# Kernel tuning notes

Hardware: AMD Instinct MI355X
Metric: run time of the kernel (lower is better)

## Reference

```python
import jax, jax.numpy as jnp
import numpy as np
from jax import lax

GN_EPS = 1e-5
LRELU_SLOPE = 0.2
TOP_K = 3
COMMITMENT = 0.25
NUM_CODES = 1024

def conv(x, w, b, stride=1, pad=1):
    y = lax.conv_general_dilated(x, w, (stride, stride), ((pad, pad), (pad, pad)),
                                 dimension_numbers=('NCHW', 'OIHW', 'NCHW'))
    return y + b[None, :, None, None]

def conv_transpose(x, w, b, stride=2, pad=1, out_pad=1):
    # torch ConvTranspose2d: w is (Cin, Cout, kH, kW); equivalent to lhs-dilated conv
    # with flipped, io-swapped kernel and padding k-1-p (plus out_pad on high side).
    k = w.shape[2]
    p = k - 1 - pad
    w_f = jnp.transpose(jnp.flip(w, (2, 3)), (1, 0, 2, 3))  # -> OIHW
    y = lax.conv_general_dilated(x, w_f, (1, 1), ((p, p + out_pad), (p, p + out_pad)),
                                 lhs_dilation=(stride, stride),
                                 dimension_numbers=('NCHW', 'OIHW', 'NCHW'))
    return y + b[None, :, None, None]

def group_norm(x, g, beta, groups=2):
    N, C, H, W = x.shape
    xg = x.reshape(N, groups, C // groups, H, W)
    mu = xg.mean((2, 3, 4), keepdims=True)
    var = xg.var((2, 3, 4), keepdims=True)
    xn = ((xg - mu) * lax.rsqrt(var + GN_EPS)).reshape(N, C, H, W)
    return xn * g[None, :, None, None] + beta[None, :, None, None]

def lrelu(x):
    return jnp.where(x >= 0, x, LRELU_SLOPE * x)

def vq_ema_eval(z, emb):
    # z: [B, D, H, W] -> tokens [N, D]; eval path (no EMA buffer updates)
    inputs = jnp.transpose(z, (0, 2, 3, 1))  # [B,H,W,D]
    flat = inputs.reshape(-1, emb.shape[1])
    d = (jnp.sum(flat ** 2, 1, keepdims=True) + jnp.sum(emb ** 2, 1)
         - 2.0 * flat @ emb.T)  # [N, K]
    _, idx = lax.top_k(-d, TOP_K)  # top_k smallest distances
    q0 = emb[idx[:, 0]].reshape(inputs.shape)
    e_latent_loss = jnp.mean((lax.stop_gradient(q0) - inputs) ** 2)
    loss = COMMITMENT * e_latent_loss
    quantized = inputs + lax.stop_gradient(q0 - inputs)  # straight-through
    # perplexity uses the LAST (k-th nearest) encodings, matching the torch loop
    last = idx[:, TOP_K - 1]
    counts = jnp.zeros((emb.shape[0],), flat.dtype).at[last].add(1.0)
    avg_probs = counts / flat.shape[0]
    perplexity = jnp.exp(-jnp.sum(avg_probs * jnp.log(avg_probs + 1e-10)))
    return loss, jnp.transpose(quantized, (0, 3, 1, 2)), perplexity

def setup_inputs() -> dict:
    key = jax.random.key(0)
    ks = jax.random.split(key, 16)
    s = 0.05
    d = {
        'x': jax.random.normal(ks[0], (4, 4, 96, 96), jnp.float32),
        'e0_w': jax.random.normal(ks[1], (128, 4, 3, 3), jnp.float32) * s,
        'e0_b': jnp.zeros((128,), jnp.float32),
        'e0_g': jnp.ones((128,), jnp.float32),
        'e0_beta': jnp.zeros((128,), jnp.float32),
        'e1_w': jax.random.normal(ks[2], (128, 128, 3, 3), jnp.float32) * s,
        'e1_b': jnp.zeros((128,), jnp.float32),
        'e1_g': jnp.ones((128,), jnp.float32),
        'e1_beta': jnp.zeros((128,), jnp.float32),
        'pv_w': jax.random.normal(ks[3], (128, 128, 1, 1), jnp.float32) * s,
        'pv_b': jnp.zeros((128,), jnp.float32),
        'emb': jax.random.normal(ks[4], (NUM_CODES, 128), jnp.float32),
        'd0_w': jax.random.normal(ks[5], (128, 128, 3, 3), jnp.float32) * s,  # ConvT: (Cin,Cout,k,k)
        'd0_b': jnp.zeros((128,), jnp.float32),
        'd0_g': jnp.ones((128,), jnp.float32),
        'd0_beta': jnp.zeros((128,), jnp.float32),
        'd1_w': jax.random.normal(ks[6], (128, 256, 3, 3), jnp.float32) * s,
        'd1_b': jnp.zeros((128,), jnp.float32),
        'd1_g': jnp.ones((128,), jnp.float32),
        'd1_beta': jnp.zeros((128,), jnp.float32),
        'proj_w': jax.random.normal(ks[7], (128, 128, 1, 1), jnp.float32) * s,
        'proj_b': jnp.zeros((128,), jnp.float32),
        'ro_w': jax.random.normal(ks[8], (4, 128, 1, 1), jnp.float32) * s,
        'ro_b': jnp.zeros((4,), jnp.float32),
    }
    return d

def reference(x, e0_w, e0_b, e0_g, e0_beta, e1_w, e1_b, e1_g, e1_beta,
              pv_w, pv_b, emb,
              d0_w, d0_b, d0_g, d0_beta, d1_w, d1_b, d1_g, d1_beta,
              proj_w, proj_b, ro_w, ro_b):
    # Encoder: strides [1, 2]
    enc1 = lrelu(group_norm(conv(x, e0_w, e0_b, stride=1, pad=1), e0_g, e0_beta))
    latent = lrelu(group_norm(conv(enc1, e1_w, e1_b, stride=2, pad=1), e1_g, e1_beta))
    z = conv(latent, pv_w, pv_b, stride=1, pad=0)
    loss, quantized, perplexity = vq_ema_eval(z, emb)
    # Decoder: strides [2, 1]; skip projected (embedding_dim != C_out)
    skip = conv(enc1, proj_w, proj_b, stride=1, pad=0)
    h = lrelu(group_norm(conv_transpose(quantized, d0_w, d0_b, stride=2, pad=1, out_pad=1), d0_g, d0_beta))
    y = lrelu(group_norm(conv(jnp.concatenate([h, skip], axis=1), d1_w, d1_b, stride=1, pad=1), d1_g, d1_beta))
    x_recon = conv(y, ro_w, ro_b, stride=1, pad=0)
    return (loss, x_recon, perplexity)
```

## Files before the change

kernel.cpp:

```cpp
#include <hip/hip_runtime.h>

#define DEVI __device__ __forceinline__

typedef unsigned short u16;
typedef __attribute__((ext_vector_type(8))) short bf8v;
typedef __attribute__((ext_vector_type(4))) short s4v;
typedef __attribute__((ext_vector_type(4))) float f4v;

constexpr int NB = 4, C = 128, H = 96, W = 96, HW = H * W;
constexpr int HL = 48, WL = 48, HWL = HL * WL;
constexpr int CODES = 1024, DIM = 128;
constexpr int ROWS = NB * HWL;

DEVI float lrelu_f(float v) { return v >= 0.f ? v : 0.2f * v; }

DEVI u16 f2bf(float f) {
  union { float f; unsigned u; } v; v.f = f;
  unsigned r = (v.u + 0x7FFFu + ((v.u >> 16) & 1u)) >> 16;
  return (u16)r;
}

DEVI float bf2f(u16 h) {
  union { unsigned u; float f; } v; v.u = (unsigned)h << 16;
  return v.f;
}

DEVI void wave_red2(float& s, float& s2) {
#pragma unroll
  for (int o = 32; o > 0; o >>= 1) { s += __shfl_down(s, o); s2 += __shfl_down(s2, o); }
}

DEVI bool block_red2(float& s, float& s2) {
  wave_red2(s, s2);
  __shared__ float ls[8], ls2[8];
  int wv = threadIdx.x >> 6, ln = threadIdx.x & 63;
  if (ln == 0) { ls[wv] = s; ls2[wv] = s2; }
  __syncthreads();
  if (threadIdx.x == 0) {
    s = ls[0] + ls[1] + ls[2] + ls[3];
    s2 = ls2[0] + ls2[1] + ls2[2] + ls2[3];
    return true;
  }
  return false;
}

DEVI void ins3(float e, int j, float& d0, int& i0, float& d1, int& i1, float& d2, int& i2) {
  bool b0 = (e < d0) || (e == d0 && j < i0);
  bool b1 = (e < d1) || (e == d1 && j < i1);
  bool b2 = (e < d2) || (e == d2 && j < i2);
  float nd0 = b0 ? e : d0;             int ni0 = b0 ? j : i0;
  float nd1 = b0 ? d0 : (b1 ? e : d1); int ni1 = b0 ? i0 : (b1 ? j : i1);
  float nd2 = b1 ? d1 : (b2 ? e : d2); int ni2 = b1 ? i1 : (b2 ? j : i2);
  d0 = nd0; i0 = ni0; d1 = nd1; i1 = ni1; d2 = nd2; i2 = ni2;
}

__global__ __launch_bounds__(256) void k_red16(const float2* __restrict__ src,
                                               float* __restrict__ dst, int per) {
  int slot = blockIdx.x;
  float s = 0.f, s2 = 0.f;
  for (int i = threadIdx.x; i < per; i += 256) {
    float2 v = src[(size_t)slot * per + i];
    s += v.x; s2 += v.y;
  }
  if (block_red2(s, s2)) { dst[slot * 2] = s; dst[slot * 2 + 1] = s2; }
}

__global__ __launch_bounds__(256) void k_pack_all(
    const float* __restrict__ d1_w, const float* __restrict__ d0_w,
    const float* __restrict__ pj_w, const float* __restrict__ emb,
    u16* __restrict__ A1, u16* __restrict__ A0, u16* __restrict__ Apj,
    u16* __restrict__ ehtil, float* __restrict__ enorm, float* __restrict__ counts) {
  int b = blockIdx.x, t = threadIdx.x;
  if (b < 1152) {
    int i = b * 256 + t;
    int ci = i & 31, co = (i >> 5) & 127, r = i >> 12;
    int kx = r % 3; int r2 = r / 3; int ch = r2 & 7, ky = r2 >> 3;
    A1[i] = f2bf(d1_w[((size_t)(co * 256 + ch * 32 + ci) * 3 + ky) * 3 + kx]);
  } else if (b < 1728) {
    int i = (b - 1152) * 256 + t;
    int ci = i & 31, co = (i >> 5) & 127, r = i >> 12;
    int wx = r % 3; int r2 = r / 3; int ch = r2 & 3, wy = r2 >> 2;
    A0[i] = f2bf(d0_w[((size_t)((ch * 32 + ci) * 128 + co) * 3 + wy) * 3 + wx]);
  } else if (b < 1792) {
    int i = (b - 1728) * 256 + t;
    int ci = i & 31, co = (i >> 5) & 127, ch = i >> 12;
    Apj[i] = f2bf(pj_w[co * 128 + ch * 32 + ci]);
  } else if (b < 1920) {
    int g = (b - 1792) * 256 + t;
    int ct = g >> 9; int rem = g & 511;
    int j = rem >> 6; int l = rem & 63;
    int code = ct * 16 + (l & 15);
    int kb = j * 32 + (l >> 4) * 8;
    bool lo = kb >= 128; int k0 = lo ? kb - 128 : kb;
    const float* ep = emb + (size_t)code * DIM + k0;
    u16 o[8];
#pragma unroll
    for (int e = 0; e < 8; ++e) {
      float v = ep[e];
      u16 h = f2bf(v);
      o[e] = lo ? f2bf(v - bf2f(h)) : h;
    }
    bf8v ov = {(short)o[0], (short)o[1], (short)o[2], (short)o[3],
               (short)o[4], (short)o[5], (short)o[6], (short)o[7]};
    *(bf8v*)&ehtil[(size_t)g * 8] = ov;
  } else if (b < 1924) {
    int e = (b - 1920) * 256 + t;
    const float4* p = (const float4*)(emb + (size_t)e * DIM);
    float s = 0.f;
#pragma unroll 8
    for (int i = 0; i < 32; ++i) {
      float4 v = p[i];
      s = fmaf(v.x, v.x, s); s = fmaf(v.y, v.y, s); s = fmaf(v.z, v.z, s); s = fmaf(v.w, v.w, s);
    }
    enorm[e] = s;
  } else {
#pragma unroll
    for (int k = 0; k < 4; ++k) counts[t + k * 256] = 0.f;
  }
}

__global__ __launch_bounds__(256) void k_conv_e0t(
    const float* __restrict__ x, const float* __restrict__ wg,
    const float* __restrict__ bias, float* __restrict__ out, float2* __restrict__ ps) {
  __shared__ float xs[4][18][104];
  int b = blockIdx.x;
  int rq = b % 6; int co = (b / 6) & 127; int n = b / 768;
  int t = threadIdx.x;
  int tx = t & 15, r = t >> 4;
  int y0 = rq * 16;
  for (int e = t; e < 4 * 18 * 104; e += 256) {
    int ci = e / 1872; int rem = e - ci * 1872;
    int row = rem / 104; int off = rem - row * 104;
    int iy = y0 - 1 + row; int ix = off - 1;
    float v = 0.f;
    if ((unsigned)iy < 96u && (unsigned)ix < 96u)
      v = x[((size_t)(n * 4 + ci)) * HW + iy * 96 + ix];
    xs[ci][row][off] = v;
  }
  float wr[4][9];
  const float* wp = wg + co * 36;
#pragma unroll
  for (int ci = 0; ci < 4; ++ci)
#pragma unroll
    for (int k = 0; k < 9; ++k) wr[ci][k] = wp[ci * 9 + k];
  float bv = bias[co];
  __syncthreads();
  float acc[6];
#pragma unroll
  for (int p = 0; p < 6; ++p) acc[p] = bv;
#pragma unroll
  for (int ci = 0; ci < 4; ++ci) {
#pragma unroll
    for (int ky = 0; ky < 3; ++ky) {
      const float* rp = &xs[ci][r + ky][6 * tx];
      float f[8];
#pragma unroll
      for (int j = 0; j < 4; ++j) {
        float2 v2 = *(const float2*)(rp + 2 * j);
        f[2 * j] = v2.x; f[2 * j + 1] = v2.y;
      }
      float w0 = wr[ci][ky * 3 + 0], w1 = wr[ci][ky * 3 + 1], w2 = wr[ci][ky * 3 + 2];
#pragma unroll
      for (int p = 0; p < 6; ++p)
        acc[p] = fmaf(w0, f[p], fmaf(w1, f[p + 1], fmaf(w2, f[p + 2], acc[p])));
    }
  }
  float* op = out + ((size_t)(n * 128 + co) * 96 + (y0 + r)) * 96 + 6 * tx;
#pragma unroll
  for (int j = 0; j < 3; ++j) {
    float2 v2 = { acc[2 * j], acc[2 * j + 1] };
    *(float2*)(op + 2 * j) = v2;
  }
  float s = 0.f, s2 = 0.f;
#pragma unroll
  for (int p = 0; p < 6; ++p) { s += acc[p]; s2 += acc[p] * acc[p]; }
  if (block_red2(s, s2)) {
    int slot = n * 2 + (co >> 6);
    ps[(size_t)slot * 384 + (co & 63) * 6 + rq] = make_float2(s, s2);
  }
}

__global__ __launch_bounds__(256) void k_gn_pad(
    const float* __restrict__ in, const float* __restrict__ stats,
    const float* __restrict__ gam, const float* __restrict__ bet, float* __restrict__ outp) {
  int idx = blockIdx.x * 256 + threadIdx.x;
  int col = idx % 100; int r2 = idx / 100; int row = r2 % 98; int c2 = r2 / 98;
  int c = c2 & 127; int n = c2 >> 7;
  float v = 0.f;
  if (row >= 1 && row <= 96 && col >= 1 && col <= 96) {
    const float* st = stats + (n * 2 + (c >> 6)) * 2;
    const float invc = 1.f / (64.f * 9216.f);
    float mu = st[0] * invc;
    float var = fmaf(-mu, mu, st[1] * invc);
    float rs = rsqrtf(var + 1e-5f);
    float raw = in[(size_t)c2 * 9216 + (row - 1) * 96 + (col - 1)];
    v = lrelu_f(fmaf((raw - mu) * rs, gam[c], bet[c]));
  }
  outp[idx] = v;
}

__global__ __launch_bounds__(256) void k_gn_nhwc_bf(
    const float* __restrict__ in, u16* __restrict__ outb, const float* __restrict__ stats,
    const float* __restrict__ gam, const float* __restrict__ bet) {
  int idx = blockIdx.x * 256 + threadIdx.x;
  int c = idx & 127;
  int n = idx / (9216 * 128);
  const float* st = stats + (n * 2 + (c >> 6)) * 2;
  const float invcnt = 1.f / (64.f * 9216.f);
  float mu = st[0] * invcnt;
  float var = fmaf(-mu, mu, st[1] * invcnt);
  float rs = rsqrtf(var + 1e-5f);
  float v = in[idx];
  outb[idx] = f2bf(lrelu_f(fmaf((v - mu) * rs, gam[c], bet[c])));
}

__global__ __launch_bounds__(256, 4) void k_conv_e1s(
    const float* __restrict__ gnpad, const float* __restrict__ wg, float* __restrict__ part) {
  __shared__ float insh[8 * 500];
  __shared__ float wsh[8 * 576];
  int b = blockIdx.x;
  int cb = b & 1; int kb = (b >> 1) & 3; int rq = (b >> 3) % 24; int n = b / 192;
  int co0 = cb * 64;
  int t = threadIdx.x;
  int tx = t & 15, r = (t >> 4) & 1, cg = t >> 5;
  float acc[8][3];
#pragma unroll
  for (int c = 0; c < 8; ++c)
#pragma unroll
    for (int p = 0; p < 3; ++p) acc[c][p] = 0.f;
  for (int cc = 0; cc < 4; ++cc) {
    __syncthreads();
    const float4* src = (const float4*)(gnpad + ((size_t)(n * 128 + kb * 32 + cc * 8)) * 9800 + 4 * rq * 100);
#pragma unroll
    for (int j = 0; j < 4; ++j) {
      int e = t + j * 256;
      if (e < 1000) {
        int ci = e / 125; int q = e - ci * 125;
        *(float4*)&insh[ci * 500 + q * 4] = src[(size_t)ci * 2450 + q];
      }
    }
#pragma unroll
    for (int j = 0; j < 18; ++j) {
      int e = t + j * 256;
      int ci = e / 576; int rem = e - ci * 576; int k = rem >> 6; int co = rem & 63;
      wsh[e] = wg[(size_t)(co0 + co) * 1152 + (kb * 32 + cc * 8 + ci) * 9 + k];
    }
    __syncthreads();
#pragma unroll
    for (int ci = 0; ci < 8; ++ci) {
      float iv[3][3][3];
      int ib = ci * 500 + (2 * r) * 100 + 2 * tx;
#pragma unroll
      for (int ky = 0; ky < 3; ++ky) {
#pragma unroll
        for (int p = 0; p < 3; ++p) {
          int a = ib + ky * 100 + 32 * p;
          float2 v2 = *(const float2*)&insh[a];
          iv[ky][p][0] = v2.x; iv[ky][p][1] = v2.y; iv[ky][p][2] = insh[a + 2];
        }
      }
#pragma unroll
      for (int k = 0; k < 9; ++k) {
        float4 wa = *(const float4*)&wsh[ci * 576 + k * 64 + cg * 8];
        float4 wb = *(const float4*)&wsh[ci * 576 + k * 64 + cg * 8 + 4];
        int ky = k / 3, kx = k - ky * 3;
#pragma unroll
        for (int p = 0; p < 3; ++p) {
          float ivv = iv[ky][p][kx];
          acc[0][p] = fmaf(wa.x, ivv, acc[0][p]);
          acc[1][p] = fmaf(wa.y, ivv, acc[1][p]);
          acc[2][p] = fmaf(wa.z, ivv, acc[2][p]);
          acc[3][p] = fmaf(wa.w, ivv, acc[3][p]);
          acc[4][p] = fmaf(wb.x, ivv, acc[4][p]);
          acc[5][p] = fmaf(wb.y, ivv, acc[5][p]);
          acc[6][p] = fmaf(wb.z, ivv, acc[6][p]);
          acc[7][p] = fmaf(wb.w, ivv, acc[7][p]);
        }
      }
    }
  }
  int oy = 2 * rq + r;
#pragma unroll
  for (int c = 0; c < 8; ++c) {
    size_t ob = (size_t)kb * 1179648 + ((size_t)(n * 128 + co0 + cg * 8 + c)) * HWL + oy * 48 + tx;
#pragma unroll
    for (int p = 0; p < 3; ++p) part[ob + 16 * p] = acc[c][p];
  }
}

__global__ __launch_bounds__(256) void k_e1comb(
    const float* __restrict__ part, const float* __restrict__ bias,
    float* __restrict__ latent, float2* __restrict__ ps) {
  int idx = blockIdx.x * 256 + threadIdx.x;
  int c = (idx / HWL) & 127;
  int n = idx / (HWL * 128);
  float v = part[idx] + part[idx + 1179648] + part[idx + 2 * 1179648] + part[idx + 3 * 1179648] + bias[c];
  latent[idx] = v;
  float s = v, s2 = v * v;
  if (block_red2(s, s2)) {
    int slot = n * 2 + (c >> 6);
    int j = blockIdx.x % 9;
    ps[(size_t)slot * 576 + (c & 63) * 9 + j] = make_float2(s, s2);
  }
}

__global__ __launch_bounds__(256, 2) void k_pv(
    const float* __restrict__ in, const float* __restrict__ w,
    const float* __restrict__ bias, const float* __restrict__ stats1,
    const float* __restrict__ gam, const float* __restrict__ bet,
    u16* __restrict__ zp) {
  int b = blockIdx.x;
  int pxb = b % 36; int cb = (b / 36) & 1; int n = b / 72;
  int t = threadIdx.x;
  int pxg = t & 7, cg = t >> 3;
  int px0 = pxb * 64 + pxg * 8;
  int cobase = cb * 64 + cg * 2;
  const float invc = 1.f / (64.f * 2304.f);
  float acc[2][8];
#pragma unroll
  for (int c = 0; c < 2; ++c) {
    float bv = bias[cobase + c];
#pragma unroll
    for (int p = 0; p < 8; ++p) acc[c][p] = bv;
  }
  const float* ipb = in + (size_t)n * 128 * HWL + px0;
  for (int ci0 = 0; ci0 < 128; ci0 += 4) {
    float inr[4][8];
#pragma unroll
    for (int i = 0; i < 4; ++i) {
      int c = ci0 + i;
      const float* st = stats1 + (n * 2 + (c >> 6)) * 2;
      float mu = st[0] * invc;
      float var = fmaf(-mu, mu, st[1] * invc);
      float rsv = rsqrtf(var + 1e-5f);
      float ga = gam[c], be = bet[c];
      const float* ip = ipb + (size_t)c * HWL;
      float4 a = *(const float4*)ip; float4 bq = *(const float4*)(ip + 4);
      inr[i][0] = lrelu_f(fmaf((a.x - mu) * rsv, ga, be));
      inr[i][1] = lrelu_f(fmaf((a.y - mu) * rsv, ga, be));
      inr[i][2] = lrelu_f(fmaf((a.z - mu) * rsv, ga, be));
      inr[i][3] = lrelu_f(fmaf((a.w - mu) * rsv, ga, be));
      inr[i][4] = lrelu_f(fmaf((bq.x - mu) * rsv, ga, be));
      inr[i][5] = lrelu_f(fmaf((bq.y - mu) * rsv, ga, be));
      inr[i][6] = lrelu_f(fmaf((bq.z - mu) * rsv, ga, be));
      inr[i][7] = lrelu_f(fmaf((bq.w - mu) * rsv, ga, be));
    }
    float wr[2][4];
#pragma unroll
    for (int c = 0; c < 2; ++c) {
      float4 wv = *(const float4*)&w[(size_t)(cobase + c) * 128 + ci0];
      wr[c][0] = wv.x; wr[c][1] = wv.y; wr[c][2] = wv.z; wr[c][3] = wv.w;
    }
#pragma unroll
    for (int i = 0; i < 4; ++i)
#pragma unroll
      for (int c = 0; c < 2; ++c)
#pragma unroll
        for (int p = 0; p < 8; ++p) acc[c][p] = fmaf(wr[c][i], inr[i][p], acc[c][p]);
  }
#pragma unroll
  for (int p = 0; p < 8; ++p) {
    size_t r = (size_t)n * HWL + px0 + p;
    u16 h0 = f2bf(acc[0][p]); u16 l0 = f2bf(acc[0][p] - bf2f(h0));
    u16 h1 = f2bf(acc[1][p]); u16 l1 = f2bf(acc[1][p] - bf2f(h1));
    unsigned hp = (unsigned)h0 | ((unsigned)h1 << 16);
    unsigned lp = (unsigned)l0 | ((unsigned)l1 << 16);
    *(unsigned*)&zp[r * 256 + cobase] = hp;
    *(unsigned*)&zp[r * 256 + 128 + cobase] = lp;
  }
}

__global__ __launch_bounds__(1024, 1) void k_vq(
    const u16* __restrict__ zp, const u16* __restrict__ ehtil,
    const float* __restrict__ emb, const float* __restrict__ enorm,
    u16* __restrict__ qb, float* __restrict__ counts, float* __restrict__ pvq) {
  __shared__ float wd[16][16][3];
  __shared__ int   wi[16][16][3];
  __shared__ float lred[16];
  __shared__ int hist[CODES];
  int r0 = blockIdx.x * 16;
  int t = threadIdx.x, w = t >> 6, lane = t & 63;
  int ln16 = lane & 15, quad = lane >> 4;
  hist[t] = 0;
  const u16* zrow = zp + (size_t)(r0 + ln16) * 256 + quad * 8;
  bf8v bh[4], bl[4];
#pragma unroll
  for (int kk = 0; kk < 4; ++kk) {
    bh[kk] = *(const bf8v*)(zrow + kk * 32);
    bl[kk] = *(const bf8v*)(zrow + 128 + kk * 32);
  }
  float d0 = 3.4e38f, d1 = 3.4e38f, d2 = 3.4e38f;
  int i0 = -1, i1 = -1, i2 = -1;
  const u16* abase = ehtil + (size_t)(w * 4) * 4096 + lane * 8;
#pragma unroll
  for (int tt = 0; tt < 4; ++tt) {
    const u16* ap = abase + tt * 4096;
    bf8v af[8];
#pragma unroll
    for (int j = 0; j < 8; ++j) af[j] = *(const bf8v*)(ap + j * 512);
    f4v accA = (f4v){0.f, 0.f, 0.f, 0.f};
    f4v accB = (f4v){0.f, 0.f, 0.f, 0.f};
    f4v accC = (f4v){0.f, 0.f, 0.f, 0.f};
#pragma unroll
    for (int kk = 0; kk < 4; ++kk) {
      accA = __builtin_amdgcn_mfma_f32_16x16x32_bf16(af[kk], bh[kk], accA, 0, 0, 0);
      accB = __builtin_amdgcn_mfma_f32_16x16x32_bf16(af[4 + kk], bh[kk], accB, 0, 0, 0);
      accC = __builtin_amdgcn_mfma_f32_16x16x32_bf16(af[kk], bl[kk], accC, 0, 0, 0);
    }
    int cbase = (w * 4 + tt) * 16 + quad * 4;
#pragma unroll
    for (int g = 0; g < 4; ++g) {
      int code = cbase + g;
      float dot = accA[g] + accB[g] + accC[g];
      float d = fmaf(-2.f, dot, enorm[code]);
      bool b0 = d < d0, b1 = d < d1, b2 = d < d2;
      float nd0 = b0 ? d : d0;             int ni0 = b0 ? code : i0;
      float nd1 = b0 ? d0 : (b1 ? d : d1); int ni1 = b0 ? i0 : (b1 ? code : i1);
      float nd2 = b1 ? d1 : (b2 ? d : d2); int ni2 = b1 ? i1 : (b2 ? code : i2);
      d0 = nd0; i0 = ni0; d1 = nd1; i1 = ni1; d2 = nd2; i2 = ni2;
    }
  }
#pragma unroll
  for (int off = 16; off <= 32; off <<= 1) {
    float e0 = __shfl_xor(d0, off), e1 = __shfl_xor(d1, off), e2 = __shfl_xor(d2, off);
    int j0 = __shfl_xor(i0, off), j1 = __shfl_xor(i1, off), j2 = __shfl_xor(i2, off);
    ins3(e0, j0, d0, i0, d1, i1, d2, i2);
    ins3(e1, j1, d0, i0, d1, i1, d2, i2);
    ins3(e2, j2, d0, i0, d1, i1, d2, i2);
  }
  if (quad == 0) {
    wd[w][ln16][0] = d0; wd[w][ln16][1] = d1; wd[w][ln16][2] = d2;
    wi[w][ln16][0] = i0; wi[w][ln16][1] = i1; wi[w][ln16][2] = i2;
  }
  __syncthreads();
  float bd; int bi;
  if (lane < 48) { bd = wd[lane / 3][w][lane % 3]; bi = wi[lane / 3][w][lane % 3]; }
  else { bd = 3.4e38f; bi = 0x7fffffff; }
  int a[3];
#pragma unroll
  for (int p = 0; p < 3; ++p) {
    float d = bd; int i = bi;
#pragma unroll
    for (int o = 1; o <= 32; o <<= 1) {
      float od = __shfl_xor(d, o); int oi = __shfl_xor(i, o);
      if (od < d || (od == d && oi < i)) { d = od; i = oi; }
    }
    a[p] = i;
    if (bi == i) { bd = 3.4e38f; bi = 0x7fffffff; }
  }
  int r = r0 + w;
  const float* q0p = emb + (size_t)a[0] * DIM;
  const u16* zr = zp + (size_t)r * 256;
  float lp = 0.f;
#pragma unroll
  for (int cc = 0; cc < 2; ++cc) {
    int c = lane + cc * 64;
    float qv = q0p[c];
    qb[(size_t)r * 128 + c] = f2bf(qv);
    float zv = bf2f(zr[c]) + bf2f(zr[128 + c]);
    float dd = zv - qv;
    lp = fmaf(dd, dd, lp);
  }
#pragma unroll
  for (int o = 32; o > 0; o >>= 1) lp += __shfl_down(lp, o);
  if (lane == 0) { lred[w] = lp; atomicAdd(&hist[a[2]], 1); }
  __syncthreads();
  if (t == 0) {
    float s = 0.f;
#pragma unroll
    for (int q = 0; q < 16; ++q) s += lred[q];
    pvq[blockIdx.x] = s;
  }
  int cnt = hist[t];
  if (cnt) atomicAdd(&counts[t], (float)cnt);
}

__global__ __launch_bounds__(256) void k_finalize(
    const float* __restrict__ counts, const float* __restrict__ pvq, float* __restrict__ out) {
  float local = 0.f;
#pragma unroll
  for (int k = 0; k < 4; ++k) {
    float cnt = counts[threadIdx.x + k * 256];
    float pr = cnt * (1.f / (float)ROWS);
    local = fmaf(pr, logf(pr + 1e-10f), local);
  }
  float lsum = 0.f;
  for (int i = threadIdx.x; i < ROWS / 16; i += 256) lsum += pvq[i];
  if (block_red2(local, lsum)) {
    out[1 + NB * 4 * HW] = expf(-local);
    out[0] = 0.25f * lsum * (1.f / (9216.f * 128.f));
  }
}

__global__ __launch_bounds__(256) void k_proj_m(
    const float* __restrict__ enc1, const u16* __restrict__ Apj,
    const float* __restrict__ bias, const float* __restrict__ stats0,
    const float* __restrict__ gam, const float* __restrict__ bet,
    u16* __restrict__ skipb) {
  __shared__ u16 Ash[128 * 32];
  __shared__ u16 Bsh[96 * 32];
  int b = blockIdx.x; int rowi = b % 96; int n = b / 96; int px0 = rowi * 96;
  int t = threadIdx.x; int w = t >> 6; int lane = t & 63;
  int ln16 = lane & 15, quad = lane >> 4;
  int co0w = (w & 1) * 64; int pxh = (w >> 1) * 48;
  int c_l = t & 31, xg = t >> 5;
  const float invc = 1.f / (64.f * 9216.f);
  f4v acc[4][3];
#pragma unroll
  for (int mt = 0; mt < 4; ++mt)
#pragma unroll
    for (int nt = 0; nt < 3; ++nt) acc[mt][nt] = (f4v){0.f, 0.f, 0.f, 0.f};
  for (int ch = 0; ch < 4; ++ch) {
    __syncthreads();
#pragma unroll
    for (int e = 0; e < 2; ++e) {
      int i = t + e * 256;
      *(bf8v*)&Ash[i * 8] = *(const bf8v*)&Apj[ch * 4096 + i * 8];
    }
    int c = ch * 32 + c_l;
    const float* st = stats0 + (n * 2 + (ch >> 1)) * 2;
    float mu = st[0] * invc;
    float var = fmaf(-mu, mu, st[1] * invc);
    float rsv = rsqrtf(var + 1e-5f);
    float ga = gam[c], be = bet[c];
    const float* ip = enc1 + (size_t)(n * 128 + c) * 9216 + px0 + xg * 12;
#pragma unroll
    for (int j4 = 0; j4 < 3; ++j4) {
      float4 v = *(const float4*)(ip + j4 * 4);
      int pxb = xg * 12 + j4 * 4;
      Bsh[(pxb + 0) * 32 + c_l] = f2bf(lrelu_f(fmaf((v.x - mu) * rsv, ga, be)));
      Bsh[(pxb + 1) * 32 + c_l] = f2bf(lrelu_f(fmaf((v.y - mu) * rsv, ga, be)));
      Bsh[(pxb + 2) * 32 + c_l] = f2bf(lrelu_f(fmaf((v.z - mu) * rsv, ga, be)));
      Bsh[(pxb + 3) * 32 + c_l] = f2bf(lrelu_f(fmaf((v.w - mu) * rsv, ga, be)));
    }
    __syncthreads();
    bf8v af[4];
#pragma unroll
    for (int mt = 0; mt < 4; ++mt)
      af[mt] = *(const bf8v*)&Ash[(co0w + mt * 16 + ln16) * 32 + quad * 8];
#pragma unroll
    for (int nt = 0; nt < 3; ++nt) {
      bf8v bfv = *(const bf8v*)&Bsh[(pxh + nt * 16 + ln16) * 32 + quad * 8];
#pragma unroll
      for (int mt = 0; mt < 4; ++mt)
        acc[mt][nt] = __builtin_amdgcn_mfma_f32_16x16x32_bf16(af[mt], bfv, acc[mt][nt], 0, 0, 0);
    }
  }
#pragma unroll
  for (int mt = 0; mt < 4; ++mt) {
    int co = co0w + mt * 16 + quad * 4;
    float4 bv = *(const float4*)&bias[co];
#pragma unroll
    for (int nt = 0; nt < 3; ++nt) {
      int px = px0 + pxh + nt * 16 + ln16;
      u16* dp = skipb + (size_t)(n * 9216 + px) * 128 + co;
      s4v sv;
      sv.x = (short)f2bf(acc[mt][nt].x + bv.x);
      sv.y = (short)f2bf(acc[mt][nt].y + bv.y);
      sv.z = (short)f2bf(acc[mt][nt].z + bv.z);
      sv.w = (short)f2bf(acc[mt][nt].w + bv.w);
      *(s4v*)dp = sv;
    }
  }
}

__global__ __launch_bounds__(256) void k_convt_d0m(
    const u16* __restrict__ qb, const u16* __restrict__ A0,
    const float* __restrict__ bias, float* __restrict__ h, float2* __restrict__ ps) {
  __shared__ u16 Ash[2 * 128 * 32];
  __shared__ u16 Bsh[49 * 32];
  int b = blockIdx.x; int rx = b & 1; int oy = (b >> 1) % 96; int n = b / 192;
  int t = threadIdx.x; int w = t >> 6; int lane = t & 63;
  int ln16 = lane & 15, quad = lane >> 4;
  int co0w = w * 32;
  f4v acc[2][3];
#pragma unroll
  for (int mt = 0; mt < 2; ++mt)
#pragma unroll
    for (int nt = 0; nt < 3; ++nt) acc[mt][nt] = (f4v){0.f, 0.f, 0.f, 0.f};
  int nyt, wys[2], iys[2];
  if (oy & 1) {
    wys[0] = 2; iys[0] = (oy - 1) >> 1;
    wys[1] = 0; iys[1] = (oy + 1) >> 1;
    nyt = (iys[1] < 48) ? 2 : 1;
  } else { wys[0] = 1; iys[0] = oy >> 1; wys[1] = 0; iys[1] = 0; nyt = 1; }
  int nxt = rx ? 2 : 1;
  int wxs[2], xof[2];
  if (rx) { wxs[0] = 2; xof[0] = 0; wxs[1] = 0; xof[1] = 1; }
  else { wxs[0] = 1; xof[0] = 0; wxs[1] = 0; xof[1] = 0; }
  for (int yt = 0; yt < nyt; ++yt) {
    for (int ch = 0; ch < 4; ++ch) {
      __syncthreads();
      for (int e = t; e < nxt * 512; e += 256) {
        int xt = e >> 9, e2 = e & 511;
        const u16* Asrc = A0 + (size_t)(((wys[yt] * 4 + ch) * 3 + wxs[xt]) * 4096);
        *(bf8v*)&Ash[xt * 4096 + e2 * 8] = *(const bf8v*)&Asrc[e2 * 8];
      }
      const u16* bbase = qb + (size_t)(n * 2304 + iys[yt] * 48) * 128 + ch * 32;
      for (int e = t; e < 196; e += 256) {
        int row = e >> 2, seg = e & 3;
        bf8v v = {0, 0, 0, 0, 0, 0, 0, 0};
        if (row < 48) v = *(const bf8v*)&bbase[row * 128 + seg * 8];
        *(bf8v*)&Bsh[row * 32 + seg * 8] = v;
      }
      __syncthreads();
      for (int xt = 0; xt < nxt; ++xt) {
        bf8v af[2];
#pragma unroll
        for (int mt = 0; mt < 2; ++mt)
          af[mt] = *(const bf8v*)&Ash[xt * 4096 + (co0w + mt * 16 + ln16) * 32 + quad * 8];
#pragma unroll
        for (int nt = 0; nt < 3; ++nt) {
          bf8v bfv = *(const bf8v*)&Bsh[(nt * 16 + ln16 + xof[xt]) * 32 + quad * 8];
#pragma unroll
          for (int mt = 0; mt < 2; ++mt)
            acc[mt][nt] = __builtin_amdgcn_mfma_f32_16x16x32_bf16(af[mt], bfv, acc[mt][nt], 0, 0, 0);
        }
      }
    }
  }
  float s = 0.f, s2 = 0.f;
#pragma unroll
  for (int mt = 0; mt < 2; ++mt) {
    int co = co0w + mt * 16 + quad * 4;
    float4 bv = *(const float4*)&bias[co];
#pragma unroll
    for (int nt = 0; nt < 3; ++nt) {
      int px = nt * 16 + ln16;
      int ox = 2 * px + rx;
      float4 v;
      v.x = acc[mt][nt].x + bv.x; v.y = acc[mt][nt].y + bv.y;
      v.z = acc[mt][nt].z + bv.z; v.w = acc[mt][nt].w + bv.w;
      *(float4*)(h + (size_t)(n * 9216 + oy * 96 + ox) * 128 + co) = v;
      s += v.x + v.y + v.z + v.w;
      s2 += v.x * v.x + v.y * v.y + v.z * v.z + v.w * v.w;
    }
  }
  wave_red2(s, s2);
  if (lane == 0) {
    int slot = n * 2 + (w >> 1);
    ps[(size_t)slot * 384 + (oy * 2 + rx) * 2 + (w & 1)] = make_float2(s, s2);
  }
}

__global__ __launch_bounds__(256) void k_conv_d1m(
    const u16* __restrict__ hb, const u16* __restrict__ sb,
    const u16* __restrict__ A1, const float* __restrict__ bias,
    float* __restrict__ y, float2* __restrict__ ps) {
  __shared__ u16 Ash[3 * 64 * 32];
  __shared__ u16 Bsh[98 * 32];
  int b = blockIdx.x; int cb = b & 1; int oy = (b >> 1) % 96; int n = b / 192;
  int t = threadIdx.x; int w = t >> 6; int lane = t & 63;
  int ln16 = lane & 15, quad = lane >> 4;
  int co0w = (w & 1) * 32; int pxh = (w >> 1) * 48;
  f4v acc[2][3];
#pragma unroll
  for (int mt = 0; mt < 2; ++mt)
#pragma unroll
    for (int nt = 0; nt < 3; ++nt) acc[mt][nt] = (f4v){0.f, 0.f, 0.f, 0.f};
  int ky0 = (oy == 0) ? 1 : 0, ky1 = (oy == 95) ? 1 : 2;
  for (int ky = ky0; ky <= ky1; ++ky) {
    int iy = oy + ky - 1;
    for (int ch = 0; ch < 8; ++ch) {
      const u16* src = (ch < 4) ? hb : sb;
      int c0 = (ch & 3) * 32;
      const u16* Asrc = A1 + (size_t)(ky * 8 + ch) * 12288;
      const u16* bbase = src + (size_t)(n * 9216 + iy * 96) * 128 + c0;
      __syncthreads();
#pragma unroll
      for (int j = 0; j < 3; ++j) {
        int e = t + j * 256;
        int kx = e >> 8; int e2 = e & 255; int co_l = e2 >> 2; int seg = e2 & 3;
        *(bf8v*)&Ash[(kx * 64 + co_l) * 32 + seg * 8] =
            *(const bf8v*)&Asrc[(size_t)kx * 4096 + (cb * 64 + co_l) * 32 + seg * 8];
      }
      for (int e = t; e < 392; e += 256) {
        int row = e >> 2, seg = e & 3;
        int ix = row - 1;
        bf8v v = {0, 0, 0, 0, 0, 0, 0, 0};
        if ((unsigned)ix < 96u) v = *(const bf8v*)&bbase[ix * 128 + seg * 8];
        *(bf8v*)&Bsh[row * 32 + seg * 8] = v;
      }
      __syncthreads();
#pragma unroll
      for (int kx = 0; kx < 3; ++kx) {
        bf8v af[2];
#pragma unroll
        for (int mt = 0; mt < 2; ++mt)
          af[mt] = *(const bf8v*)&Ash[(kx * 64 + co0w + mt * 16 + ln16) * 32 + quad * 8];
#pragma unroll
        for (int nt = 0; nt < 3; ++nt) {
          bf8v bfv = *(const bf8v*)&Bsh[(pxh + nt * 16 + ln16 + kx) * 32 + quad * 8];
#pragma unroll
          for (int mt = 0; mt < 2; ++mt)
            acc[mt][nt] = __builtin_amdgcn_mfma_f32_16x16x32_bf16(af[mt], bfv, acc[mt][nt], 0, 0, 0);
        }
      }
    }
  }
  float s = 0.f, s2 = 0.f;
#pragma unroll
  for (int mt = 0; mt < 2; ++mt) {
    int co = cb * 64 + co0w + mt * 16 + quad * 4;
    float4 bv = *(const float4*)&bias[co];
#pragma unroll
    for (int nt = 0; nt < 3; ++nt) {
      int px = pxh + nt * 16 + ln16;
      float4 v;
      v.x = acc[mt][nt].x + bv.x; v.y = acc[mt][nt].y + bv.y;
      v.z = acc[mt][nt].z + bv.z; v.w = acc[mt][nt].w + bv.w;
      *(float4*)(y + (size_t)(n * 9216 + oy * 96 + px) * 128 + co) = v;
      s += v.x + v.y + v.z + v.w;
      s2 += v.x * v.x + v.y * v.y + v.z * v.z + v.w * v.w;
    }
  }
  wave_red2(s, s2);
  if (lane == 0) {
    int slot = n * 2 + cb;
    ps[(size_t)slot * 384 + oy * 4 + w] = make_float2(s, s2);
  }
}

__global__ __launch_bounds__(256) void k_ro(
    const float* __restrict__ y, const float* __restrict__ w,
    const float* __restrict__ bias, const float* __restrict__ stats3,
    const float* __restrict__ gam, const float* __restrict__ bet,
    float* __restrict__ out) {
  __shared__ float wsh[512];
  __shared__ float gsh[128], bsh[128];
  __shared__ float red[64][16];
  int b = blockIdx.x; int n = b / 144; int px0 = (b % 144) * 64;
  int t = threadIdx.x; int q = t & 3, pxl = t >> 2;
  for (int e = t; e < 512; e += 256) wsh[e] = w[e];
  if (t < 128) { gsh[t] = gam[t]; bsh[t] = bet[t]; }
  __syncthreads();
  const float invc = 1.f / (64.f * 9216.f);
  int g = q >> 1;
  const float* st = stats3 + (n * 2 + g) * 2;
  float mu = st[0] * invc;
  float var = fmaf(-mu, mu, st[1] * invc);
  float rsv = rsqrtf(var + 1e-5f);
  const float* yb = y + (size_t)(n * 9216 + px0 + pxl) * 128 + q * 32;
  float s0 = 0.f, s1 = 0.f, s2 = 0.f, s3 = 0.f;
#pragma unroll
  for (int j = 0; j < 8; ++j) {
    float4 v = *(const float4*)(yb + j * 4);
    int c0 = q * 32 + j * 4;
    float vx = lrelu_f(fmaf((v.x - mu) * rsv, gsh[c0 + 0], bsh[c0 + 0]));
    float vy = lrelu_f(fmaf((v.y - mu) * rsv, gsh[c0 + 1], bsh[c0 + 1]));
    float vz = lrelu_f(fmaf((v.z - mu) * rsv, gsh[c0 + 2], bsh[c0 + 2]));
    float vw = lrelu_f(fmaf((v.w - mu) * rsv, gsh[c0 + 3], bsh[c0 + 3]));
    const float* w0 = &wsh[0 * 128 + c0];
    const float* w1 = &wsh[1 * 128 + c0];
    const float* w2 = &wsh[2 * 128 + c0];
    const float* w3 = &wsh[3 * 128 + c0];
    s0 += vx * w0[0] + vy * w0[1] + vz * w0[2] + vw * w0[3];
    s1 += vx * w1[0] + vy * w1[1] + vz * w1[2] + vw * w1[3];
    s2 += vx * w2[0] + vy * w2[1] + vz * w2[2] + vw * w2[3];
    s3 += vx * w3[0] + vy * w3[1] + vz * w3[2] + vw * w3[3];
  }
  red[pxl][q * 4 + 0] = s0; red[pxl][q * 4 + 1] = s1;
  red[pxl][q * 4 + 2] = s2; red[pxl][q * 4 + 3] = s3;
  __syncthreads();
  float val = red[pxl][0 * 4 + q] + red[pxl][1 * 4 + q] + red[pxl][2 * 4 + q] + red[pxl][3 * 4 + q] + bias[q];
  out[1 + (size_t)(n * 4 + q) * 9216 + px0 + pxl] = val;
}

extern "C" void kernel_launch(void* const* d_in, const int* in_sizes, int n_in,
                              void* d_out, int out_size, void* d_ws, size_t ws_size,
                              hipStream_t stream) {
  (void)in_sizes; (void)n_in; (void)out_size; (void)ws_size;
  const float* x     = (const float*)d_in[0];
  const float* e0_w  = (const float*)d_in[1];
  const float* e0_b  = (const float*)d_in[2];
  const float* e0_g  = (const float*)d_in[3];
  const float* e0_bt = (const float*)d_in[4];
  const float* e1_w  = (const float*)d_in[5];
  const float* e1_b  = (const float*)d_in[6];
  const float* e1_g  = (const float*)d_in[7];
  const float* e1_bt = (const float*)d_in[8];
  const float* pv_w  = (const float*)d_in[9];
  const float* pv_b  = (const float*)d_in[10];
  const float* emb   = (const float*)d_in[11];
  const float* d0_w  = (const float*)d_in[12];
  const float* d0_b  = (const float*)d_in[13];
  const float* d0_g  = (const float*)d_in[14];
  const float* d0_bt = (const float*)d_in[15];
  const float* d1_w  = (const float*)d_in[16];
  const float* d1_b  = (const float*)d_in[17];
  const float* d1_g  = (const float*)d_in[18];
  const float* d1_bt = (const float*)d_in[19];
  const float* pj_w  = (const float*)d_in[20];
  const float* pj_b  = (const float*)d_in[21];
  const float* ro_w  = (const float*)d_in[22];
  const float* ro_b  = (const float*)d_in[23];
  float* out = (float*)d_out;
  float* ws = (float*)d_ws;

  float* stats  = ws;
  float* counts = ws + 64;
  float* enorm  = ws + 1088;
  float* pvq    = ws + 2112;
  float2* ps_e0 = (float2*)(ws + 3264);
  float2* ps_e1 = (float2*)(ws + 76992);
  float2* ps_d0 = (float2*)(ws + 95424);
  float2* ps_d1 = (float2*)(ws + 107712);
  float* enc1   = ws + 114688;
  float* latent = enc1 + (size_t)NB * C * HW;
  float* zbuf   = latent + (size_t)NB * C * HWL;
  float* hy     = zbuf + (size_t)NB * C * HWL;
  u16* qb    = (u16*)(hy + (size_t)NB * C * HW);
  u16* hb    = qb + (size_t)NB * C * HWL;
  u16* skipb = hb + (size_t)NB * C * HW;
  u16* A1    = skipb + (size_t)NB * C * HW;
  u16* A0    = A1 + 294912;
  u16* Apj   = A0 + 147456;
  u16* ehtil = Apj + 16384 + 64;
  u16* zp    = (u16*)zbuf;
  float* gnpad = (float*)qb;

  k_pack_all<<<1925, 256, 0, stream>>>(d1_w, d0_w, pj_w, emb, A1, A0, Apj, ehtil, enorm, counts);

  k_conv_e0t<<<3072, 256, 0, stream>>>(x, e0_w, e0_b, enc1, ps_e0);
  k_red16<<<8, 256, 0, stream>>>(ps_e0, stats + 0, 384);
  k_gn_pad<<<512 * 9800 / 256, 256, 0, stream>>>(enc1, stats + 0, e0_g, e0_bt, gnpad);
  k_conv_e1s<<<768, 256, 0, stream>>>(gnpad, e1_w, hy);
  k_e1comb<<<NB * C * HWL / 256, 256, 0, stream>>>(hy, e1_b, latent, ps_e1);
  k_red16<<<8, 256, 0, stream>>>(ps_e1, stats + 16, 576);
  k_pv<<<288, 256, 0, stream>>>(latent, pv_w, pv_b, stats + 16, e1_g, e1_bt, zp);
  k_vq<<<ROWS / 16, 1024, 0, stream>>>(zp, ehtil, emb, enorm, qb, counts, pvq);
  k_finalize<<<1, 256, 0, stream>>>(counts, pvq, out);

  k_proj_m<<<NB * 96, 256, 0, stream>>>(enc1, Apj, pj_b, stats + 0, e0_g, e0_bt, skipb);
  k_convt_d0m<<<NB * 96 * 2, 256, 0, stream>>>(qb, A0, d0_b, hy, ps_d0);
  k_red16<<<8, 256, 0, stream>>>(ps_d0, stats + 32, 384);
  k_gn_nhwc_bf<<<NB * C * HW / 256, 256, 0, stream>>>(hy, hb, stats + 32, d0_g, d0_bt);
  k_conv_d1m<<<NB * 96 * 2, 256, 0, stream>>>(hb, skipb, A1, d1_b, hy, ps_d1);
  k_red16<<<8, 256, 0, stream>>>(ps_d1, stats + 48, 384);
  k_ro<<<NB * 144, 256, 0, stream>>>(hy, ro_w, ro_b, stats + 48, d1_g, d1_bt, out);
}
```

Baseline: 384.0 us.

## Move encoder stride-2 conv to split-bf16 MFMA with packed NHWC input

Replaces the FP32 split-K direct conv for the second encoder layer, and its separate combine kernel, with an MFMA kernel. Precision is kept by splitting values into hi/lo bf16 parts and issuing three MFMAs per product. The group-norm pass now writes channel-blocked, even/odd-column-deinterleaved bf16 hi/lo rows, and weights are pre-packed in the pack kernel. Bias, the latent store and the partial statistics are fused into the conv epilogue, which removes the partial-sum buffer traffic and one launch. The cost is three times the MFMA work plus rounding error from the split-bf16 approximation.

```diff
diff --git a/kernel.cpp b/kernel.cpp
--- a/kernel.cpp
+++ b/kernel.cpp
@@ -68,8 +68,10 @@
 __global__ __launch_bounds__(256) void k_pack_all(
     const float* __restrict__ d1_w, const float* __restrict__ d0_w,
     const float* __restrict__ pj_w, const float* __restrict__ emb,
+    const float* __restrict__ e1_w,
     u16* __restrict__ A1, u16* __restrict__ A0, u16* __restrict__ Apj,
-    u16* __restrict__ ehtil, float* __restrict__ enorm, float* __restrict__ counts) {
+    u16* __restrict__ ehtil, u16* __restrict__ We1,
+    float* __restrict__ enorm, float* __restrict__ counts) {
   int b = blockIdx.x, t = threadIdx.x;
   if (b < 1152) {
     int i = b * 256 + t;
@@ -113,9 +115,27 @@
       s = fmaf(v.x, v.x, s); s = fmaf(v.y, v.y, s); s = fmaf(v.z, v.z, s); s = fmaf(v.w, v.w, s);
     }
     enorm[e] = s;
+  } else if (b == 1924) {
+#pragma unroll
+    for (int k = 0; k < 4; ++k) counts[t + k * 256] = 0.f;
   } else {
-#pragma unroll
-    for (int k = 0; k < 4; ++k) counts[t + k * 256] = 0.f;
+    int p = (b - 1925) * 256 + t;
+    int s = p >> 6, l = p & 63;
+    int ct = s & 7; int r = s >> 3;
+    int kx = r % 3; int r2 = r / 3; int ch = r2 & 3, ky = r2 >> 2;
+    int co = ct * 16 + (l & 15), ci0 = ch * 32 + (l >> 4) * 8;
+    u16 hh[8], ll[8];
+#pragma unroll
+    for (int e = 0; e < 8; ++e) {
+      float v = e1_w[((size_t)(co * 128 + ci0 + e) * 3 + ky) * 3 + kx];
+      u16 h = f2bf(v); hh[e] = h; ll[e] = f2bf(v - bf2f(h));
+    }
+    bf8v hv = {(short)hh[0], (short)hh[1], (short)hh[2], (short)hh[3],
+               (short)hh[4], (short)hh[5], (short)hh[6], (short)hh[7]};
+    bf8v lv = {(short)ll[0], (short)ll[1], (short)ll[2], (short)ll[3],
+               (short)ll[4], (short)ll[5], (short)ll[6], (short)ll[7]};
+    *(bf8v*)&We1[(size_t)s * 1024 + l * 8] = hv;
+    *(bf8v*)&We1[(size_t)s * 1024 + 512 + l * 8] = lv;
   }
 }
 
@@ -180,23 +200,116 @@
   }
 }
 
-__global__ __launch_bounds__(256) void k_gn_pad(
-    const float* __restrict__ in, const float* __restrict__ stats,
-    const float* __restrict__ gam, const float* __restrict__ bet, float* __restrict__ outp) {
-  int idx = blockIdx.x * 256 + threadIdx.x;
-  int col = idx % 100; int r2 = idx / 100; int row = r2 % 98; int c2 = r2 / 98;
-  int c = c2 & 127; int n = c2 >> 7;
-  float v = 0.f;
-  if (row >= 1 && row <= 96 && col >= 1 && col <= 96) {
-    const float* st = stats + (n * 2 + (c >> 6)) * 2;
-    const float invc = 1.f / (64.f * 9216.f);
-    float mu = st[0] * invc;
-    float var = fmaf(-mu, mu, st[1] * invc);
-    float rs = rsqrtf(var + 1e-5f);
-    float raw = in[(size_t)c2 * 9216 + (row - 1) * 96 + (col - 1)];
-    v = lrelu_f(fmaf((raw - mu) * rs, gam[c], bet[c]));
-  }
-  outp[idx] = v;
+__global__ __launch_bounds__(256) void k_gn_px(
+    const float* __restrict__ enc1, const float* __restrict__ stats,
+    const float* __restrict__ gam, const float* __restrict__ bet, u16* __restrict__ xp) {
+  int b = blockIdx.x;
+  int ch = b & 3; int iy = (b >> 2) % 96; int n = b / 384;
+  int t = threadIdx.x;
+  const float invc = 1.f / (64.f * 9216.f);
+  size_t chunk = ((size_t)((n * 96 + iy) * 4 + ch)) * 6208;
+  for (int e = t; e < 388; e += 256) {
+    int oct = e / 97, u = e - oct * 97;
+    int ix = (u < 48) ? 2 * u : 2 * (u - 48) - 1;
+    u16* dh = xp + chunk + u * 32 + oct * 8;
+    u16* dl = dh + 3104;
+    if (ix < 0) {
+      bf8v z = {0, 0, 0, 0, 0, 0, 0, 0};
+      *(bf8v*)dh = z; *(bf8v*)dl = z;
+      continue;
+    }
+    u16 hh[8], ll[8];
+#pragma unroll
+    for (int e8 = 0; e8 < 8; ++e8) {
+      int c = ch * 32 + oct * 8 + e8;
+      const float* st = stats + (n * 2 + (c >> 6)) * 2;
+      float mu = st[0] * invc;
+      float var = fmaf(-mu, mu, st[1] * invc);
+      float rs = rsqrtf(var + 1e-5f);
+      float raw = enc1[((size_t)(n * 128 + c)) * 9216 + iy * 96 + ix];
+      float v = lrelu_f(fmaf((raw - mu) * rs, gam[c], bet[c]));
+      u16 h = f2bf(v); hh[e8] = h; ll[e8] = f2bf(v - bf2f(h));
+    }
+    bf8v hv = {(short)hh[0], (short)hh[1], (short)hh[2], (short)hh[3],
+               (short)hh[4], (short)hh[5], (short)hh[6], (short)hh[7]};
+    bf8v lv = {(short)ll[0], (short)ll[1], (short)ll[2], (short)ll[3],
+               (short)ll[4], (short)ll[5], (short)ll[6], (short)ll[7]};
+    *(bf8v*)dh = hv; *(bf8v*)dl = lv;
+  }
+}
+
+__global__ __launch_bounds__(256) void k_conv_e1m(
+    const u16* __restrict__ xp, const u16* __restrict__ We1,
+    const float* __restrict__ bias, float* __restrict__ latent, float2* __restrict__ ps) {
+  __shared__ u16 Bsh[2 * 97 * 36];
+  __shared__ float ls[4], ls2[4];
+  int b = blockIdx.x; int cb = b & 1; int oy = (b >> 1) % 48; int n = b / 96;
+  int t = threadIdx.x; int w = t >> 6; int lane = t & 63;
+  int ln16 = lane & 15, quad = lane >> 4;
+  int ctg = cb * 4 + w;
+  f4v acc[3];
+#pragma unroll
+  for (int nt = 0; nt < 3; ++nt) acc[nt] = (f4v){0.f, 0.f, 0.f, 0.f};
+  for (int ky = 0; ky < 3; ++ky) {
+    int iy = 2 * oy + ky - 1;
+    for (int ch = 0; ch < 4; ++ch) {
+      __syncthreads();
+      if ((unsigned)iy < 96u) {
+        const u16* src = xp + ((size_t)((n * 96 + iy) * 4 + ch)) * 6208;
+        for (int e = t; e < 776; e += 256) {
+          int h = e / 388; int rem = e - h * 388; int oct = rem / 97; int u = rem - oct * 97;
+          *(bf8v*)&Bsh[(h * 97 + u) * 36 + oct * 8] = *(const bf8v*)&src[h * 3104 + u * 32 + oct * 8];
+        }
+      } else {
+        bf8v z = {0, 0, 0, 0, 0, 0, 0, 0};
+        for (int e = t; e < 776; e += 256) {
+          int h = e / 388; int rem = e - h * 388; int oct = rem / 97; int u = rem - oct * 97;
+          *(bf8v*)&Bsh[(h * 97 + u) * 36 + oct * 8] = z;
+        }
+      }
+      __syncthreads();
+      const u16* wb = We1 + ((size_t)((ky * 4 + ch) * 3)) * 8192;
+#pragma unroll
+      for (int kx = 0; kx < 3; ++kx) {
+        const u16* sl = wb + (kx * 8 + ctg) * 1024 + lane * 8;
+        bf8v ah = *(const bf8v*)sl;
+        bf8v al = *(const bf8v*)(sl + 512);
+#pragma unroll
+        for (int nt = 0; nt < 3; ++nt) {
+          int px = nt * 16 + ln16;
+          int u = (kx == 1) ? px : (48 + px + (kx >> 1));
+          const u16* bb = &Bsh[u * 36 + quad * 8];
+          bf8v bh = *(const bf8v*)bb;
+          bf8v bl = *(const bf8v*)(bb + 3492);
+          acc[nt] = __builtin_amdgcn_mfma_f32_16x16x32_bf16(ah, bh, acc[nt], 0, 0, 0);
+          acc[nt] = __builtin_amdgcn_mfma_f32_16x16x32_bf16(al, bh, acc[nt], 0, 0, 0);
+          acc[nt] = __builtin_amdgcn_mfma_f32_16x16x32_bf16(ah, bl, acc[nt], 0, 0, 0);
+        }
+      }
+    }
+  }
+  int co0 = cb * 64 + w * 16 + quad * 4;
+  float4 bv = *(const float4*)&bias[co0];
+  float s = 0.f, s2 = 0.f;
+#pragma unroll
+  for (int nt = 0; nt < 3; ++nt) {
+    int px = nt * 16 + ln16;
+#pragma unroll
+    for (int g = 0; g < 4; ++g) {
+      float bvg = (g == 0) ? bv.x : (g == 1) ? bv.y : (g == 2) ? bv.z : bv.w;
+      float v = acc[nt][g] + bvg;
+      latent[((size_t)(n * 128 + co0 + g)) * 2304 + oy * 48 + px] = v;
+      s += v; s2 += v * v;
+    }
+  }
+  wave_red2(s, s2);
+  if (lane == 0) { ls[w] = s; ls2[w] = s2; }
+  __syncthreads();
+  if (t == 0) {
+    int slot = n * 2 + cb;
+    ps[(size_t)slot * 48 + oy] =
+        make_float2(ls[0] + ls[1] + ls[2] + ls[3], ls2[0] + ls2[1] + ls2[2] + ls2[3]);
+  }
 }
 
 __global__ __launch_bounds__(256) void k_gn_nhwc_bf(
@@ -212,96 +325,6 @@
   float rs = rsqrtf(var + 1e-5f);
   float v = in[idx];
   outb[idx] = f2bf(lrelu_f(fmaf((v - mu) * rs, gam[c], bet[c])));
-}
-
-__global__ __launch_bounds__(256, 4) void k_conv_e1s(
-    const float* __restrict__ gnpad, const float* __restrict__ wg, float* __restrict__ part) {
-  __shared__ float insh[8 * 500];
-  __shared__ float wsh[8 * 576];
-  int b = blockIdx.x;
-  int cb = b & 1; int kb = (b >> 1) & 3; int rq = (b >> 3) % 24; int n = b / 192;
-  int co0 = cb * 64;
-  int t = threadIdx.x;
-  int tx = t & 15, r = (t >> 4) & 1, cg = t >> 5;
-  float acc[8][3];
-#pragma unroll
-  for (int c = 0; c < 8; ++c)
-#pragma unroll
-    for (int p = 0; p < 3; ++p) acc[c][p] = 0.f;
-  for (int cc = 0; cc < 4; ++cc) {
-    __syncthreads();
-    const float4* src = (const float4*)(gnpad + ((size_t)(n * 128 + kb * 32 + cc * 8)) * 9800 + 4 * rq * 100);
-#pragma unroll
-    for (int j = 0; j < 4; ++j) {
-      int e = t + j * 256;
-      if (e < 1000) {
-        int ci = e / 125; int q = e - ci * 125;
-        *(float4*)&insh[ci * 500 + q * 4] = src[(size_t)ci * 2450 + q];
-      }
-    }
-#pragma unroll
-    for (int j = 0; j < 18; ++j) {
-      int e = t + j * 256;
-      int ci = e / 576; int rem = e - ci * 576; int k = rem >> 6; int co = rem & 63;
-      wsh[e] = wg[(size_t)(co0 + co) * 1152 + (kb * 32 + cc * 8 + ci) * 9 + k];
-    }
-    __syncthreads();
-#pragma unroll
-    for (int ci = 0; ci < 8; ++ci) {
-      float iv[3][3][3];
-      int ib = ci * 500 + (2 * r) * 100 + 2 * tx;
-#pragma unroll
-      for (int ky = 0; ky < 3; ++ky) {
-#pragma unroll
-        for (int p = 0; p < 3; ++p) {
-          int a = ib + ky * 100 + 32 * p;
-          float2 v2 = *(const float2*)&insh[a];
-          iv[ky][p][0] = v2.x; iv[ky][p][1] = v2.y; iv[ky][p][2] = insh[a + 2];
-        }
-      }
-#pragma unroll
-      for (int k = 0; k < 9; ++k) {
-        float4 wa = *(const float4*)&wsh[ci * 576 + k * 64 + cg * 8];
-        float4 wb = *(const float4*)&wsh[ci * 576 + k * 64 + cg * 8 + 4];
-        int ky = k / 3, kx = k - ky * 3;
-#pragma unroll
-        for (int p = 0; p < 3; ++p) {
-          float ivv = iv[ky][p][kx];
-          acc[0][p] = fmaf(wa.x, ivv, acc[0][p]);
-          acc[1][p] = fmaf(wa.y, ivv, acc[1][p]);
-          acc[2][p] = fmaf(wa.z, ivv, acc[2][p]);
-          acc[3][p] = fmaf(wa.w, ivv, acc[3][p]);
-          acc[4][p] = fmaf(wb.x, ivv, acc[4][p]);
-          acc[5][p] = fmaf(wb.y, ivv, acc[5][p]);
-          acc[6][p] = fmaf(wb.z, ivv, acc[6][p]);
-          acc[7][p] = fmaf(wb.w, ivv, acc[7][p]);
-        }
-      }
-    }
-  }
-  int oy = 2 * rq + r;
-#pragma unroll
-  for (int c = 0; c < 8; ++c) {
-    size_t ob = (size_t)kb * 1179648 + ((size_t)(n * 128 + co0 + cg * 8 + c)) * HWL + oy * 48 + tx;
-#pragma unroll
-    for (int p = 0; p < 3; ++p) part[ob + 16 * p] = acc[c][p];
-  }
-}
-
-__global__ __launch_bounds__(256) void k_e1comb(
-    const float* __restrict__ part, const float* __restrict__ bias,
-    float* __restrict__ latent, float2* __restrict__ ps) {
-  int idx = blockIdx.x * 256 + threadIdx.x;
-  int c = (idx / HWL) & 127;
-  int n = idx / (HWL * 128);
-  float v = part[idx] + part[idx + 1179648] + part[idx + 2 * 1179648] + part[idx + 3 * 1179648] + bias[c];
-  latent[idx] = v;
-  float s = v, s2 = v * v;
-  if (block_red2(s, s2)) {
-    int slot = n * 2 + (c >> 6);
-    int j = blockIdx.x % 9;
-    ps[(size_t)slot * 576 + (c & 63) * 9 + j] = make_float2(s, s2);
-  }
 }
 
 __global__ __launch_bounds__(256, 2) void k_pv(
@@ -817,16 +840,17 @@
   u16* Apj   = A0 + 147456;
   u16* ehtil = Apj + 16384 + 64;
   u16* zp    = (u16*)zbuf;
-  float* gnpad = (float*)qb;
-
-  k_pack_all<<<1925, 256, 0, stream>>>(d1_w, d0_w, pj_w, emb, A1, A0, Apj, ehtil, enorm, counts);
+  u16* xp  = qb;
+  u16* We1 = qb + 9535488;
+
+  k_pack_all<<<2069, 256, 0, stream>>>(d1_w, d0_w, pj_w, emb, e1_w,
+                                       A1, A0, Apj, ehtil, We1, enorm, counts);
 
   k_conv_e0t<<<3072, 256, 0, stream>>>(x, e0_w, e0_b, enc1, ps_e0);
   k_red16<<<8, 256, 0, stream>>>(ps_e0, stats + 0, 384);
-  k_gn_pad<<<512 * 9800 / 256, 256, 0, stream>>>(enc1, stats + 0, e0_g, e0_bt, gnpad);
-  k_conv_e1s<<<768, 256, 0, stream>>>(gnpad, e1_w, hy);
-  k_e1comb<<<NB * C * HWL / 256, 256, 0, stream>>>(hy, e1_b, latent, ps_e1);
-  k_red16<<<8, 256, 0, stream>>>(ps_e1, stats + 16, 576);
+  k_gn_px<<<NB * 96 * 4, 256, 0, stream>>>(enc1, stats + 0, e0_g, e0_bt, xp);
+  k_conv_e1m<<<NB * 48 * 2, 256, 0, stream>>>(xp, We1, e1_b, latent, ps_e1);
+  k_red16<<<8, 256, 0, stream>>>(ps_e1, stats + 16, 48);
   k_pv<<<288, 256, 0, stream>>>(latent, pv_w, pv_b, stats + 16, e1_g, e1_bt, zp);
   k_vq<<<ROWS / 16, 1024, 0, stream>>>(zp, ehtil, emb, enorm, qb, counts, pvq);
   k_finalize<<<1, 256, 0, stream>>>(counts, pvq, out);
```

After: 385.7 us. Within noise of the previous version (+0.4%).
